# Optimization experiments

Measured on AMD Instinct MI355X. Metric: run time of the kernel, lower is better.

The kernel has to match this reference:

```python
import jax, jax.numpy as jnp
import numpy as np


def setup_inputs() -> dict:
    key = jax.random.key(0)
    ks = jax.random.split(key, 7)
    B, L, D, H = 256, 1024, 768, 768
    x = jax.random.normal(ks[0], (B, L, D), dtype=jnp.float32)
    label_mask = jax.random.randint(ks[1], (B, L), 0, 2).astype(jnp.int32)
    global_prototype_tensor = jax.random.normal(ks[2], (L + 1, D), dtype=jnp.float32)
    W_h = jax.random.normal(ks[3], (H, D), dtype=jnp.float32) * 0.02
    b_h = jax.random.normal(ks[4], (H,), dtype=jnp.float32) * 0.02
    W_p = jax.random.normal(ks[5], (D, H), dtype=jnp.float32) * 0.02
    b_p = jax.random.normal(ks[6], (D,), dtype=jnp.float32) * 0.02
    return {"x": x, "label_mask": label_mask,
            "global_prototype_tensor": global_prototype_tensor,
            "W_h": W_h, "b_h": b_h, "W_p": W_p, "b_p": b_p}


def _mlp(v, W_h, b_h, W_p, b_p):
    # torch Linear: y = v @ W.T + b
    h = jax.nn.relu(jnp.einsum('ld,hd->lh', v, W_h) + b_h)
    return jnp.einsum('lh,dh->ld', h, W_p) + b_p


def reference(x, label_mask, global_prototype_tensor, W_h, b_h, W_p, b_p):
    # x: [B, L, D]; label_mask: [B, L] (1 if label i in example's label_list)
    m = label_mask.astype(x.dtype)                        # [B, L]
    pos_cnt = m.sum(0)                                    # [L]
    B = x.shape[0]
    anti_cnt = B - pos_cnt                                # [L]
    pos_sum = jnp.einsum('bl,bld->ld', m, x)              # masked segment-sum
    tot_sum = x.sum(0)                                    # [L, D]
    anti_sum = tot_sum - pos_sum

    pos_mean = pos_sum / jnp.maximum(pos_cnt, 1.0)[:, None]
    anti_mean = anti_sum / jnp.maximum(anti_cnt, 1.0)[:, None]

    avg_pos = 0.5 * pos_mean + 0.5 * global_prototype_tensor[:-1]   # [L, D]
    avg_anti = 0.5 * anti_mean + 0.5 * global_prototype_tensor[-1]  # [L, D]

    proto = _mlp(avg_pos, W_h, b_h, W_p, b_p)
    proto = jnp.where((pos_cnt > 0)[:, None], proto, 0.0)           # rows stay zero if no members

    anti_proto = _mlp(avg_anti, W_h, b_h, W_p, b_p)
    w = (anti_cnt > 0).astype(x.dtype)                              # [L]
    anti = jnp.einsum('l,ld->d', w, anti_proto) / jnp.maximum(w.sum(), 1.0)

    return jnp.concatenate([proto, anti[None, :]], axis=0)          # [L+1, D]
```

## Files before the change

### kernel.cpp

```cpp
#include <hip/hip_runtime.h>

#define L_DIM 1024
#define B_DIM 256
#define D_DIM 768
#define K_DIM 768
#define NTILES (K_DIM / 32)
#define WN    (768 * 768)

typedef _Float16 half8 __attribute__((ext_vector_type(8)));
typedef float    floatx4 __attribute__((ext_vector_type(4)));

__device__ __forceinline__ ushort f2h(float f) {
    _Float16 h = (_Float16)f;
    return __builtin_bit_cast(ushort, h);
}

__device__ __forceinline__ void gl16(const ushort* g, ushort* l) {
    __builtin_amdgcn_global_load_lds(
        (const __attribute__((address_space(1))) unsigned int*)g,
        (__attribute__((address_space(3))) unsigned int*)l, 16, 0, 0);
}

__global__ __launch_bounds__(768)
void reduce_and_cast(const float* __restrict__ x,
                     const int* __restrict__ mask,
                     const float* __restrict__ gpt,
                     const float* __restrict__ Wh, const float* __restrict__ Wp,
                     ushort* __restrict__ Vh,
                     ushort* __restrict__ WhH, ushort* __restrict__ WpH,
                     float* __restrict__ pos_cnt, unsigned* __restrict__ counter)
{
    const int tid = threadIdx.x;

    if (blockIdx.x >= 256) {
        const int idx = ((blockIdx.x - 256) * 768 + tid) * 4;
        const float4 v = (idx < WN) ? *(const float4*)(Wh + idx)
                                    : *(const float4*)(Wp + (idx - WN));
        ushort4 o;
        o.x = f2h(v.x); o.y = f2h(v.y); o.z = f2h(v.z); o.w = f2h(v.w);
        if (idx < WN) *(ushort4*)(WhH + idx) = o;
        else          *(ushort4*)(WpH + (idx - WN)) = o;
        return;
    }

    if (blockIdx.x == 0 && tid == 0) *counter = 0u;

    __shared__ int mS[256][4];
    const int l0 = blockIdx.x * 4;
    if (tid < 256)
        *(int4*)&mS[tid][0] = *(const int4*)(mask + (size_t)tid * L_DIM + l0);
    __syncthreads();

    const int row = tid / 192;
    const int t   = tid % 192;
    const int d0  = t * 4;
    const int l   = l0 + row;

    const size_t bstride = (size_t)L_DIM * D_DIM;
    const float* xp = x + (size_t)l * D_DIM + d0;

    floatx4 pos = {0.f, 0.f, 0.f, 0.f};
    floatx4 tot = {0.f, 0.f, 0.f, 0.f};
    float cnt = 0.f;

    #pragma unroll 16
    for (int b = 0; b < B_DIM; ++b) {
        const floatx4 v = __builtin_nontemporal_load((const floatx4*)(xp + (size_t)b * bstride));
        const float fm = (float)mS[b][row];
        tot += v;
        pos[0] = fmaf(fm, v[0], pos[0]);
        pos[1] = fmaf(fm, v[1], pos[1]);
        pos[2] = fmaf(fm, v[2], pos[2]);
        pos[3] = fmaf(fm, v[3], pos[3]);
        cnt += fm;
    }

    const float inv_p = 0.5f / fmaxf(cnt, 1.0f);
    const float inv_a = 0.5f / fmaxf((float)B_DIM - cnt, 1.0f);

    const float4 g4  = *(const float4*)(gpt + (size_t)l * D_DIM + d0);
    const float4 gl4 = *(const float4*)(gpt + (size_t)L_DIM * D_DIM + d0);

    ushort4 ph, ah;
    ph.x = f2h(pos[0] * inv_p + 0.5f * g4.x);
    ph.y = f2h(pos[1] * inv_p + 0.5f * g4.y);
    ph.z = f2h(pos[2] * inv_p + 0.5f * g4.z);
    ph.w = f2h(pos[3] * inv_p + 0.5f * g4.w);
    ah.x = f2h((tot[0] - pos[0]) * inv_a + 0.5f * gl4.x);
    ah.y = f2h((tot[1] - pos[1]) * inv_a + 0.5f * gl4.y);
    ah.z = f2h((tot[2] - pos[2]) * inv_a + 0.5f * gl4.z);
    ah.w = f2h((tot[3] - pos[3]) * inv_a + 0.5f * gl4.w);

    *(ushort4*)(Vh + (size_t)l * D_DIM + d0) = ph;
    *(ushort4*)(Vh + (size_t)(L_DIM + l) * D_DIM + d0) = ah;

    if (t == 0) pos_cnt[l] = cnt;
}

template<int MODE>
__global__ __launch_bounds__(256)
void gemm_f16(const ushort* __restrict__ A, const ushort* __restrict__ B,
              const float* __restrict__ bias,
              ushort* __restrict__ OutH, float* __restrict__ OutF,
              float* __restrict__ Partial,
              const float* __restrict__ cnt, unsigned* __restrict__ counter)
{
    __shared__ ushort lds[2][8192];
    __shared__ float  colsum[4][64];
    __shared__ float  red[256];
    __shared__ unsigned lastflag;

    const int tid  = threadIdx.x;
    const int lane = tid & 63;
    const int wid  = tid >> 6;
    const int brow = blockIdx.y * 128;
    const int bcol = blockIdx.x * 128;
    const int wr   = (wid >> 1) * 64;
    const int wc   = (wid & 1) * 64;

    const int srow = tid >> 2;
    const int slot = tid & 3;
    const int sk   = (slot ^ ((srow >> 1) & 3)) * 8;

    const ushort* pA0 = A + (size_t)(brow + srow) * K_DIM + sk;
    const ushort* pA1 = A + (size_t)(brow + 64 + srow) * K_DIM + sk;
    const ushort* pB0 = B + (size_t)(bcol + srow) * K_DIM + sk;
    const ushort* pB1 = B + (size_t)(bcol + 64 + srow) * K_DIM + sk;

    const int ldst = tid * 8;

    const int q   = lane >> 4;
    const int r15 = lane & 15;
    const int swz = ((q ^ ((r15 >> 1) & 3)) << 3);
    const int fA  = (wr + r15) * 32 + swz;
    const int fB  = 4096 + (wc + r15) * 32 + swz;

    floatx4 acc[4][4] = {};

    gl16(pA0, &lds[0][ldst]);
    gl16(pA1, &lds[0][2048 + ldst]);
    gl16(pB0, &lds[0][4096 + ldst]);
    gl16(pB1, &lds[0][6144 + ldst]);
    __syncthreads();

    for (int t = 0; t < NTILES; ++t) {
        const int cur = t & 1;
        if (t + 1 < NTILES) {
            const int ko = (t + 1) * 32;
            const int nxt = cur ^ 1;
            gl16(pA0 + ko, &lds[nxt][ldst]);
            gl16(pA1 + ko, &lds[nxt][2048 + ldst]);
            gl16(pB0 + ko, &lds[nxt][4096 + ldst]);
            gl16(pB1 + ko, &lds[nxt][6144 + ldst]);
        }
        half8 a[4], b[4];
        #pragma unroll
        for (int i = 0; i < 4; ++i) {
            a[i] = *(half8*)&lds[cur][fA + i * 512];
            b[i] = *(half8*)&lds[cur][fB + i * 512];
        }
        #pragma unroll
        for (int mi = 0; mi < 4; ++mi)
            #pragma unroll
            for (int ni = 0; ni < 4; ++ni)
                acc[mi][ni] = __builtin_amdgcn_mfma_f32_16x16x32_f16(a[mi], b[ni], acc[mi][ni], 0, 0, 0);
        __syncthreads();
    }

    if (MODE == 0 || brow < L_DIM) {
        #pragma unroll
        for (int mi = 0; mi < 4; ++mi) {
            #pragma unroll
            for (int ni = 0; ni < 4; ++ni) {
                const int col   = bcol + wc + ni * 16 + r15;
                const int rbase = brow + wr + mi * 16 + (q << 2);
                const float bv = bias[col];
                #pragma unroll
                for (int r = 0; r < 4; ++r) {
                    const float v = acc[mi][ni][r] + bv;
                    const int row = rbase + r;
                    if (MODE == 0) {
                        OutH[(size_t)row * D_DIM + col] = f2h(fmaxf(v, 0.f));
                    } else {
                        OutF[(size_t)row * D_DIM + col] = (cnt[row] > 0.f) ? v : 0.f;
                    }
                }
            }
        }
    } else {
        float s[4] = {0.f, 0.f, 0.f, 0.f};
        #pragma unroll
        for (int mi = 0; mi < 4; ++mi) {
            const int rbase = brow + wr + mi * 16 + (q << 2);
            #pragma unroll
            for (int r = 0; r < 4; ++r) {
                const float w = (cnt[rbase + r - L_DIM] < 255.5f) ? 1.0f : 0.0f;
                #pragma unroll
                for (int ni = 0; ni < 4; ++ni) {
                    const int col = bcol + wc + ni * 16 + r15;
                    s[ni] = fmaf(w, acc[mi][ni][r] + bias[col], s[ni]);
                }
            }
        }
        #pragma unroll
        for (int ni = 0; ni < 4; ++ni) {
            s[ni] += __shfl_down(s[ni], 32);
            s[ni] += __shfl_down(s[ni], 16);
            if (lane < 16) colsum[wid][ni * 16 + lane] = s[ni];
        }
        __syncthreads();
        if (tid < 128) {
            const float v = (tid < 64)
                ? colsum[0][tid] + colsum[2][tid]
                : colsum[1][tid - 64] + colsum[3][tid - 64];
            Partial[(size_t)(blockIdx.y - 8) * D_DIM + bcol + tid] = v;
        }
        __threadfence();
        __syncthreads();
        if (tid == 0) lastflag = (atomicAdd(counter, 1u) == 47u) ? 1u : 0u;
        __syncthreads();
        if (lastflag) {
            __threadfence();
            float w = 0.f;
            for (int i = tid; i < L_DIM; i += 256)
                w += (cnt[i] < 255.5f) ? 1.0f : 0.0f;
            red[tid] = w;
            __syncthreads();
            for (int st = 128; st > 0; st >>= 1) {
                if (tid < st) red[tid] += red[tid + st];
                __syncthreads();
            }
            const float wsum = fmaxf(red[0], 1.0f);
            #pragma unroll
            for (int j = 0; j < 3; ++j) {
                const int d = tid + j * 256;
                float sm = 0.f;
                #pragma unroll
                for (int pp = 0; pp < 8; ++pp)
                    sm += Partial[(size_t)pp * D_DIM + d];
                OutF[(size_t)L_DIM * D_DIM + d] = sm / wsum;
            }
        }
    }
}

extern "C" void kernel_launch(void* const* d_in, const int* in_sizes, int n_in,
                              void* d_out, int out_size, void* d_ws, size_t ws_size,
                              hipStream_t stream) {
    const float* x    = (const float*)d_in[0];
    const int*   mask = (const int*)d_in[1];
    const float* gpt  = (const float*)d_in[2];
    const float* W_h  = (const float*)d_in[3];
    const float* b_h  = (const float*)d_in[4];
    const float* W_p  = (const float*)d_in[5];
    const float* b_p  = (const float*)d_in[6];
    float* out = (float*)d_out;

    char* p = (char*)d_ws;
    ushort* Vh   = (ushort*)p; p += (size_t)2 * L_DIM * D_DIM * 2;
    ushort* Hh   = (ushort*)p; p += (size_t)2 * L_DIM * D_DIM * 2;
    ushort* WhH  = (ushort*)p; p += (size_t)WN * 2;
    ushort* WpH  = (ushort*)p; p += (size_t)WN * 2;
    float*  Part = (float*)p;  p += (size_t)8 * D_DIM * 4;
    float*  cnt  = (float*)p;  p += (size_t)L_DIM * 4;
    unsigned* counter = (unsigned*)p;

    reduce_and_cast<<<640, 768, 0, stream>>>(x, mask, gpt, W_h, W_p,
                                             Vh, WhH, WpH, cnt, counter);

    dim3 ggrid(D_DIM / 128, 2 * L_DIM / 128);
    gemm_f16<0><<<ggrid, 256, 0, stream>>>(Vh, WhH, b_h,
                                           Hh, nullptr, nullptr, nullptr, nullptr);
    gemm_f16<1><<<ggrid, 256, 0, stream>>>(Hh, WpH, b_p,
                                           nullptr, out, Part, cnt, counter);
}
```

Measured before the change: 176.9 us.

## Fuse both MLP GEMMs into one launch with per-row-block flags; halve reduce blocks

Merges the two GEMM launches into one 192-block kernel. The second-layer blocks spin on a per-row-block counter that the first-layer blocks increment after writing their hidden tile, so layer-2 work can start before all of layer 1 finishes and one launch is saved. The reduce kernel now uses 384-thread blocks covering 2 rows each, doubling block count for better occupancy and latency hiding over the large x read. The spin-wait relies on all first-layer blocks being scheduled before or alongside the waiting blocks, which adds deadlock risk if residency is limited.

```diff
diff --git a/kernel.cpp b/kernel.cpp
--- a/kernel.cpp
+++ b/kernel.cpp
@@ -21,19 +21,20 @@
         (__attribute__((address_space(3))) unsigned int*)l, 16, 0, 0);
 }
 
-__global__ __launch_bounds__(768)
+__global__ __launch_bounds__(384)
 void reduce_and_cast(const float* __restrict__ x,
                      const int* __restrict__ mask,
                      const float* __restrict__ gpt,
                      const float* __restrict__ Wh, const float* __restrict__ Wp,
                      ushort* __restrict__ Vh,
                      ushort* __restrict__ WhH, ushort* __restrict__ WpH,
-                     float* __restrict__ pos_cnt, unsigned* __restrict__ counter)
+                     float* __restrict__ pos_cnt,
+                     unsigned* __restrict__ counter, unsigned* __restrict__ rowcnt)
 {
     const int tid = threadIdx.x;
 
-    if (blockIdx.x >= 256) {
-        const int idx = ((blockIdx.x - 256) * 768 + tid) * 4;
+    if (blockIdx.x >= 512) {
+        const int idx = ((blockIdx.x - 512) * 384 + tid) * 4;
         const float4 v = (idx < WN) ? *(const float4*)(Wh + idx)
                                     : *(const float4*)(Wp + (idx - WN));
         ushort4 o;
@@ -43,12 +44,15 @@
         return;
     }
 
-    if (blockIdx.x == 0 && tid == 0) *counter = 0u;
-
-    __shared__ int mS[256][4];
-    const int l0 = blockIdx.x * 4;
+    if (blockIdx.x == 0) {
+        if (tid == 0) *counter = 0u;
+        if (tid < 16) rowcnt[tid] = 0u;
+    }
+
+    __shared__ int mS[256][2];
+    const int l0 = blockIdx.x * 2;
     if (tid < 256)
-        *(int4*)&mS[tid][0] = *(const int4*)(mask + (size_t)tid * L_DIM + l0);
+        *(int2*)&mS[tid][0] = *(const int2*)(mask + (size_t)tid * L_DIM + l0);
     __syncthreads();
 
     const int row = tid / 192;
@@ -97,35 +101,52 @@
     if (t == 0) pos_cnt[l] = cnt;
 }
 
-template<int MODE>
 __global__ __launch_bounds__(256)
-void gemm_f16(const ushort* __restrict__ A, const ushort* __restrict__ B,
-              const float* __restrict__ bias,
-              ushort* __restrict__ OutH, float* __restrict__ OutF,
-              float* __restrict__ Partial,
-              const float* __restrict__ cnt, unsigned* __restrict__ counter)
+void gemm_fused(const ushort* __restrict__ Vh, const ushort* __restrict__ WhH,
+                const float* __restrict__ b_h,
+                ushort* __restrict__ Hh, const ushort* __restrict__ WpH,
+                const float* __restrict__ b_p,
+                float* __restrict__ OutF, float* __restrict__ Partial,
+                const float* __restrict__ cnt,
+                unsigned* __restrict__ counter, unsigned* __restrict__ rowcnt)
 {
     __shared__ ushort lds[2][8192];
     __shared__ float  colsum[4][64];
     __shared__ float  red[256];
     __shared__ unsigned lastflag;
 
-    const int tid  = threadIdx.x;
-    const int lane = tid & 63;
-    const int wid  = tid >> 6;
-    const int brow = blockIdx.y * 128;
-    const int bcol = blockIdx.x * 128;
-    const int wr   = (wid >> 1) * 64;
-    const int wc   = (wid & 1) * 64;
+    const int tid   = threadIdx.x;
+    const int lane  = tid & 63;
+    const int wid   = tid >> 6;
+    const bool first = blockIdx.x < 96;
+    const int bid   = first ? blockIdx.x : blockIdx.x - 96;
+    const int cx    = bid % 6;
+    const int ry    = bid / 6;
+    const int brow  = ry * 128;
+    const int bcol  = cx * 128;
+    const int wr    = (wid >> 1) * 64;
+    const int wc    = (wid & 1) * 64;
+
+    const ushort* Amat = first ? Vh  : Hh;
+    const ushort* Bmat = first ? WhH : WpH;
+    const float*  bias = first ? b_h : b_p;
+
+    if (!first) {
+        if (tid == 0) {
+            while (atomicAdd(&rowcnt[ry], 0u) < 6u) { __builtin_amdgcn_s_sleep(8); }
+        }
+        __syncthreads();
+        __threadfence();
+    }
 
     const int srow = tid >> 2;
     const int slot = tid & 3;
     const int sk   = (slot ^ ((srow >> 1) & 3)) * 8;
 
-    const ushort* pA0 = A + (size_t)(brow + srow) * K_DIM + sk;
-    const ushort* pA1 = A + (size_t)(brow + 64 + srow) * K_DIM + sk;
-    const ushort* pB0 = B + (size_t)(bcol + srow) * K_DIM + sk;
-    const ushort* pB1 = B + (size_t)(bcol + 64 + srow) * K_DIM + sk;
+    const ushort* pA0 = Amat + (size_t)(brow + srow) * K_DIM + sk;
+    const ushort* pA1 = Amat + (size_t)(brow + 64 + srow) * K_DIM + sk;
+    const ushort* pB0 = Bmat + (size_t)(bcol + srow) * K_DIM + sk;
+    const ushort* pB1 = Bmat + (size_t)(bcol + 64 + srow) * K_DIM + sk;
 
     const int ldst = tid * 8;
 
@@ -167,7 +188,25 @@
         __syncthreads();
     }
 
-    if (MODE == 0 || brow < L_DIM) {
+    if (first) {
+        #pragma unroll
+        for (int mi = 0; mi < 4; ++mi) {
+            #pragma unroll
+            for (int ni = 0; ni < 4; ++ni) {
+                const int col   = bcol + wc + ni * 16 + r15;
+                const int rbase = brow + wr + mi * 16 + (q << 2);
+                const float bv = bias[col];
+                #pragma unroll
+                for (int r = 0; r < 4; ++r)
+                    Hh[(size_t)(rbase + r) * D_DIM + col] = f2h(fmaxf(acc[mi][ni][r] + bv, 0.f));
+            }
+        }
+        __syncthreads();
+        if (tid == 0) {
+            __threadfence();
+            atomicAdd(&rowcnt[ry], 1u);
+        }
+    } else if (brow < L_DIM) {
         #pragma unroll
         for (int mi = 0; mi < 4; ++mi) {
             #pragma unroll
@@ -177,13 +216,9 @@
                 const float bv = bias[col];
                 #pragma unroll
                 for (int r = 0; r < 4; ++r) {
-                    const float v = acc[mi][ni][r] + bv;
                     const int row = rbase + r;
-                    if (MODE == 0) {
-                        OutH[(size_t)row * D_DIM + col] = f2h(fmaxf(v, 0.f));
-                    } else {
-                        OutF[(size_t)row * D_DIM + col] = (cnt[row] > 0.f) ? v : 0.f;
-                    }
+                    OutF[(size_t)row * D_DIM + col] =
+                        (cnt[row] > 0.f) ? (acc[mi][ni][r] + bv) : 0.f;
                 }
             }
         }
@@ -213,7 +248,7 @@
             const float v = (tid < 64)
                 ? colsum[0][tid] + colsum[2][tid]
                 : colsum[1][tid - 64] + colsum[3][tid - 64];
-            Partial[(size_t)(blockIdx.y - 8) * D_DIM + bcol + tid] = v;
+            Partial[(size_t)(ry - 8) * D_DIM + bcol + tid] = v;
         }
         __threadfence();
         __syncthreads();
@@ -263,14 +298,12 @@
     ushort* WpH  = (ushort*)p; p += (size_t)WN * 2;
     float*  Part = (float*)p;  p += (size_t)8 * D_DIM * 4;
     float*  cnt  = (float*)p;  p += (size_t)L_DIM * 4;
-    unsigned* counter = (unsigned*)p;
-
-    reduce_and_cast<<<640, 768, 0, stream>>>(x, mask, gpt, W_h, W_p,
-                                             Vh, WhH, WpH, cnt, counter);
-
-    dim3 ggrid(D_DIM / 128, 2 * L_DIM / 128);
-    gemm_f16<0><<<ggrid, 256, 0, stream>>>(Vh, WhH, b_h,
-                                           Hh, nullptr, nullptr, nullptr, nullptr);
-    gemm_f16<1><<<ggrid, 256, 0, stream>>>(Hh, WpH, b_p,
-                                           nullptr, out, Part, cnt, counter);
-}
+    unsigned* counter = (unsigned*)p; p += 64;
+    unsigned* rowcnt  = (unsigned*)p;
+
+    reduce_and_cast<<<1280, 384, 0, stream>>>(x, mask, gpt, W_h, W_p,
+                                              Vh, WhH, WpH, cnt, counter, rowcnt);
+
+    gemm_fused<<<192, 256, 0, stream>>>(Vh, WhH, b_h, Hh, WpH, b_p,
+                                        out, Part, cnt, counter, rowcnt);
+}
```

Result: slower. 194.8 us (+10.1%).
